# Performance work log

Hardware: AMD Instinct MI355X
Metric: run time of the kernel (lower is better)

Reference implementation:

```python
import jax, jax.numpy as jnp
import numpy as np

DIM = 512
NUM_HEADS = 8
HEAD_DIM = DIM // NUM_HEADS
GAMMA = 1.0


def setup_inputs() -> dict:
    key = jax.random.key(0)
    ks = jax.random.split(key, 10)
    B, S = 2, 2048
    x_real = jax.random.normal(ks[0], (B, S, DIM), dtype=jnp.float32)
    x_imag = jax.random.normal(ks[1], (B, S, DIM), dtype=jnp.float32)
    def xavier(k, fan_in, fan_out):
        lim = float(np.sqrt(6.0 / (fan_in + fan_out)))
        return jax.random.uniform(k, (fan_in, fan_out), jnp.float32, -lim, lim)
    # torch Linear(in,out): weight [out,in]; we store transposed [in,out]
    Wq = xavier(ks[2], 2 * DIM, DIM); bq = jnp.zeros((DIM,), jnp.float32)
    Wk = xavier(ks[3], 2 * DIM, DIM); bk = jnp.zeros((DIM,), jnp.float32)
    Wv = xavier(ks[4], 2 * DIM, DIM); bv = jnp.zeros((DIM,), jnp.float32)
    Wo = xavier(ks[5], DIM, 2 * DIM); bo = jnp.zeros((2 * DIM,), jnp.float32)
    return {"x_real": x_real, "x_imag": x_imag, "Wq": Wq, "bq": bq,
            "Wk": Wk, "bk": bk, "Wv": Wv, "bv": bv, "Wo": Wo, "bo": bo}


def reference(x_real, x_imag, Wq, bq, Wk, bk, Wv, bv, Wo, bo):
    B, S, _ = x_real.shape
    real_embed = jnp.concatenate([x_real, x_imag], axis=-1)  # [B,S,2*dim]
    def proj(W, b):
        y = real_embed @ W + b                               # [B,S,dim]
        return y.reshape(B, S, NUM_HEADS, HEAD_DIM).transpose(0, 2, 1, 3)  # [B,H,S,d]
    Q = proj(Wq, bq)
    K = proj(Wk, bk)
    V = proj(Wv, bv)
    # softmax over head_dim is broadcast-invariant, so the Bhattacharyya
    # coefficient sum_d sqrt(p_i[d]*q_j[d]) factorizes into a matmul.
    sp = jnp.sqrt(jax.nn.softmax(Q, axis=-1))  # [B,H,S,d]
    sq = jnp.sqrt(jax.nn.softmax(K, axis=-1))  # [B,H,S,d]
    bc = jnp.einsum('bhid,bhjd->bhij', sp, sq)  # Bhattacharyya coeff [B,H,S,S]
    bc = jnp.clip(bc, -1.0, 1.0)
    dist = jnp.arccos(bc)
    attn = jax.nn.softmax(-GAMMA * dist * dist, axis=-1)  # [B,H,S,S]
    attended = jnp.einsum('bhij,bhjd->bhid', attn, V)
    attended = attended.transpose(0, 2, 1, 3).reshape(B, S, DIM)
    out = attended @ Wo + bo  # [B,S,2*dim] = concat(real_out, imag_out)
    return out
```

## Files before the change

kernel.cpp:

```cpp
#include <hip/hip_runtime.h>
#include <math.h>


typedef __attribute__((ext_vector_type(8))) short short8;
typedef __attribute__((ext_vector_type(4))) short bf16x4;
typedef __attribute__((ext_vector_type(4))) float f32x4;

#define MFMA(a, b, c) __builtin_amdgcn_mfma_f32_16x16x32_bf16((a), (b), (c), 0, 0, 0)

static __device__ __forceinline__ short f2bf(float f) {
    unsigned u = __float_as_uint(f);
    u += 0x7fffu + ((u >> 16) & 1u);
    return (short)(u >> 16);
}

static __device__ __forceinline__ void gld_lds16(const short* g, short* l) {
    __builtin_amdgcn_global_load_lds(
        (const __attribute__((address_space(1))) unsigned int*)g,
        (__attribute__((address_space(3))) unsigned int*)l, 16, 0, 0);
}

__global__ __launch_bounds__(256) void convert_x(
    const float* __restrict__ xr, const float* __restrict__ xi,
    short* __restrict__ xb)
{
    int idx = blockIdx.x * 256 + threadIdx.x;
    int e = idx << 2;
    int m = e >> 10, k = e & 1023;
    const float* src = (k < 512) ? xr : xi;
    float4 t = *(const float4*)(src + (size_t)m * 512 + (k & 511));
    unsigned lo = (unsigned short)f2bf(t.x) | ((unsigned)(unsigned short)f2bf(t.y) << 16);
    unsigned hi = (unsigned short)f2bf(t.z) | ((unsigned)(unsigned short)f2bf(t.w) << 16);
    uint2 o; o.x = lo; o.y = hi;
    *(uint2*)(xb + e) = o;
}

__global__ __launch_bounds__(256) void transpose_w(
    const float* __restrict__ Wq, const float* __restrict__ Wk,
    const float* __restrict__ Wv, const float* __restrict__ Wo,
    short* __restrict__ wqt, short* __restrict__ wkt,
    short* __restrict__ wvt, short* __restrict__ wot)
{
    __shared__ float t[32][33];
    const int z = blockIdx.z;
    const float* src = (z == 0) ? Wq : (z == 1) ? Wk : (z == 2) ? Wv : Wo;
    short* dst = (z == 0) ? wqt : (z == 1) ? wkt : (z == 2) ? wvt : wot;
    const int K = (z < 3) ? 1024 : 512;
    const int N = (z < 3) ? 512 : 1024;
    const int n0 = blockIdx.x << 5, k0 = blockIdx.y << 5;
    if (n0 >= N || k0 >= K) return;
    const int tx = threadIdx.x & 31, ty = threadIdx.x >> 5;
    #pragma unroll
    for (int i = 0; i < 4; ++i)
        t[ty + 8 * i][tx] = src[(size_t)(k0 + ty + 8 * i) * N + n0 + tx];
    __syncthreads();
    #pragma unroll
    for (int i = 0; i < 4; ++i)
        dst[(size_t)(n0 + ty + 8 * i) * K + k0 + tx] = f2bf(t[tx][ty + 8 * i]);
}

__global__ __launch_bounds__(128, 4) void qkv_mfma(
    const short* __restrict__ xb, const short* __restrict__ wcat,
    const float* __restrict__ bq, const float* __restrict__ bk,
    const float* __restrict__ bv,
    short* __restrict__ sp, short* __restrict__ sq, short* __restrict__ vt)
{
    __shared__ short As[2][128 * 32];
    __shared__ short Bs[2][64 * 32];
    const int jb = blockIdx.x;
    const int m0 = blockIdx.y << 7;
    const int tid = threadIdx.x;
    const int w = tid >> 6, lane = tid & 63;
    const int l = lane & 15, quad = lane >> 4;

    const int srow = lane >> 2;
    const int sseg = (lane & 3) << 3;
    const short* gA = xb   + (size_t)(m0        + (w << 6) + srow) * 1024 + sseg;
    const short* gB = wcat + (size_t)((jb << 6) + (w << 5) + srow) * 1024 + sseg;

    #pragma unroll
    for (int t = 0; t < 4; ++t)
        gld_lds16(gA + t * 16 * 1024, &As[0][((w << 2) + t) << 9]);
    #pragma unroll
    for (int t = 0; t < 2; ++t)
        gld_lds16(gB + t * 16 * 1024, &Bs[0][((w << 1) + t) << 9]);
    __syncthreads();

    const f32x4 z4 = {0.f, 0.f, 0.f, 0.f};
    f32x4 acc[4][4];
    #pragma unroll
    for (int i = 0; i < 4; ++i)
        #pragma unroll
        for (int j = 0; j < 4; ++j) acc[i][j] = z4;

    for (int kt = 0; kt < 32; ++kt) {
        const int cb = kt & 1, nb = cb ^ 1;
        if (kt < 31) {
            const int k0 = (kt + 1) << 5;
            #pragma unroll
            for (int t = 0; t < 4; ++t)
                gld_lds16(gA + k0 + t * 16 * 1024, &As[nb][((w << 2) + t) << 9]);
            #pragma unroll
            for (int t = 0; t < 2; ++t)
                gld_lds16(gB + k0 + t * 16 * 1024, &Bs[nb][((w << 1) + t) << 9]);
        }
        const short* Al = &As[cb][(w << 6) << 5];
        const short* Bl = &Bs[cb][0];
        short8 af[4], bfr[4];
        #pragma unroll
        for (int i = 0; i < 4; ++i)
            af[i] = *(const short8*)(Al + (((i << 4) + l) << 5) + (quad << 3));
        #pragma unroll
        for (int j = 0; j < 4; ++j)
            bfr[j] = *(const short8*)(Bl + (((j << 4) + l) << 5) + (quad << 3));
        #pragma unroll
        for (int i = 0; i < 4; ++i)
            #pragma unroll
            for (int j = 0; j < 4; ++j)
                acc[i][j] = MFMA(af[i], bfr[j], acc[i][j]);
        __syncthreads();
    }

    const int op = jb >> 3;
    const int h  = jb & 7;

    if (op < 2) {
        short* dst = (op == 0) ? sp : sq;
        const float* bias = (op == 0) ? bq : bk;
        float bcol[4];
        #pragma unroll
        for (int nt = 0; nt < 4; ++nt) bcol[nt] = bias[(h << 6) + (nt << 4) + l];
        #pragma unroll
        for (int i = 0; i < 4; ++i) {
            #pragma unroll
            for (int reg = 0; reg < 4; ++reg) {
                const int r = m0 + (w << 6) + (i << 4) + (quad << 2) + reg;
                const int b = r >> 11, s = r & 2047;
                float v[4];
                #pragma unroll
                for (int nt = 0; nt < 4; ++nt) v[nt] = acc[i][nt][reg] + bcol[nt];
                float mx = fmaxf(fmaxf(v[0], v[1]), fmaxf(v[2], v[3]));
                #pragma unroll
                for (int msk = 1; msk < 16; msk <<= 1) mx = fmaxf(mx, __shfl_xor(mx, msk));
                float e[4], ssum = 0.f;
                #pragma unroll
                for (int nt = 0; nt < 4; ++nt) { e[nt] = __expf(v[nt] - mx); ssum += e[nt]; }
                #pragma unroll
                for (int msk = 1; msk < 16; msk <<= 1) ssum += __shfl_xor(ssum, msk);
                float inv = 1.0f / ssum;
                short* o = dst + ((size_t)((b << 3) + h) * 2048 + s) * 64 + l;
                #pragma unroll
                for (int nt = 0; nt < 4; ++nt)
                    o[nt << 4] = f2bf(sqrtf(e[nt] * inv));
            }
        }
    } else {
        float bcol[4];
        #pragma unroll
        for (int nt = 0; nt < 4; ++nt) bcol[nt] = bv[(h << 6) + (nt << 4) + l];
        #pragma unroll
        for (int i = 0; i < 4; ++i) {
            const int sb = m0 + (w << 6) + (i << 4) + (quad << 2);
            const int b = sb >> 11, s = sb & 2047;
            #pragma unroll
            for (int nt = 0; nt < 4; ++nt) {
                const int d = (nt << 4) + l;
                bf16x4 pk;
                #pragma unroll
                for (int reg = 0; reg < 4; ++reg)
                    pk[reg] = f2bf(acc[i][nt][reg] + bcol[nt]);
                *(bf16x4*)(vt + ((size_t)((b << 3) + h) * 64 + d) * 2048 + s) = pk;
            }
        }
    }
}

__global__ __launch_bounds__(256, 4) void attn_mfma(
    const short* __restrict__ sp, const short* __restrict__ sq,
    const short* __restrict__ vt, short* __restrict__ attB)
{
    __shared__ short sqT[2][64 * 72];
    __shared__ short vtT[2][64 * 72];
    __shared__ short Pb[4][16 * 72];
    __shared__ float denB[4][16];
    const int bh = blockIdx.y;
    const int m0 = blockIdx.x << 6;
    const int tid = threadIdx.x;
    const int w = tid >> 6, lane = tid & 63;
    const int l = lane & 15, quad = lane >> 4;

    const short* spB = sp + (size_t)bh * 2048 * 64;
    const short* sqB = sq + (size_t)bh * 2048 * 64;
    const short* vtB = vt + (size_t)bh * 64 * 2048;

    const short* apr = spB + (size_t)(m0 + w * 16 + l) * 64 + quad * 8;
    short8 aq0 = *(const short8*)(apr);
    short8 aq1 = *(const short8*)(apr + 32);

    const int srow = tid >> 2;
    const int scol = (tid & 3) * 16;
    const short* sqG = sqB + (size_t)srow * 64 + scol;
    const short* vtG = vtB + (size_t)srow * 2048 + scol;
    const int ldsOff = srow * 72 + scol;

    {
        short8 a0 = *(const short8*)(sqG);
        short8 a1 = *(const short8*)(sqG + 8);
        short8 b0 = *(const short8*)(vtG);
        short8 b1 = *(const short8*)(vtG + 8);
        *(short8*)(&sqT[0][ldsOff])     = a0;
        *(short8*)(&sqT[0][ldsOff + 8]) = a1;
        *(short8*)(&vtT[0][ldsOff])     = b0;
        *(short8*)(&vtT[0][ldsOff + 8]) = b1;
    }
    __syncthreads();

    const f32x4 z4 = {0.f, 0.f, 0.f, 0.f};
    f32x4 acc[4] = {z4, z4, z4, z4};
    float den = 0.f;
    short* Pw = &Pb[w][0];

    #pragma unroll 1
    for (int jt = 0; jt < 32; ++jt) {
        const int cb = jt & 1, nb = cb ^ 1;
        const int j0n = ((jt + 1) & 31) << 6;
        short8 na0 = *(const short8*)(sqG + (size_t)j0n * 64);
        short8 na1 = *(const short8*)(sqG + (size_t)j0n * 64 + 8);
        short8 nb0 = *(const short8*)(vtG + j0n);
        short8 nb1 = *(const short8*)(vtG + j0n + 8);

        const short* sqL = &sqT[cb][0];
        #pragma unroll
        for (int nt = 0; nt < 4; ++nt) {
            const short* ar = sqL + (nt * 16 + l) * 72 + quad * 8;
            short8 sa0 = *(const short8*)(ar);
            short8 sa1 = *(const short8*)(ar + 32);
            f32x4 p = MFMA(sa0, aq0, z4);
            p = MFMA(sa1, aq1, p);
            float wv[4];
            #pragma unroll
            for (int reg = 0; reg < 4; ++reg) {
                float u = fmaxf(1.0f - p[reg], 0.0f);
                float t = 0.000922f;
                t = fmaf(t, u, 0.00152228f);
                t = fmaf(t, u, 0.00384801f);
                t = fmaf(t, u, 0.01015873f);
                t = fmaf(t, u, 0.02857143f);
                t = fmaf(t, u, 0.08888889f);
                t = fmaf(t, u, 0.33333333f);
                t = fmaf(t, u, 2.0f);
                float e = __expf(-u * t);
                wv[reg] = e;
                den += e;
            }
            uint2 pk;
            pk.x = (__float_as_uint(wv[0]) >> 16) | (__float_as_uint(wv[1]) & 0xffff0000u);
            pk.y = (__float_as_uint(wv[2]) >> 16) | (__float_as_uint(wv[3]) & 0xffff0000u);
            *(uint2*)(&Pw[l * 72 + nt * 16 + quad * 4]) = pk;
        }

        const short* pr = Pw + l * 72 + quad * 8;
        short8 pa0 = *(const short8*)(pr);
        short8 pa1 = *(const short8*)(pr + 32);
        const short* vL = &vtT[cb][0];
        #pragma unroll
        for (int t4 = 0; t4 < 4; ++t4) {
            const short* vr = vL + (t4 * 16 + l) * 72 + quad * 8;
            short8 vb0 = *(const short8*)(vr);
            short8 vb1 = *(const short8*)(vr + 32);
            acc[t4] = MFMA(pa0, vb0, acc[t4]);
            acc[t4] = MFMA(pa1, vb1, acc[t4]);
        }

        *(short8*)(&sqT[nb][ldsOff])     = na0;
        *(short8*)(&sqT[nb][ldsOff + 8]) = na1;
        *(short8*)(&vtT[nb][ldsOff])     = nb0;
        *(short8*)(&vtT[nb][ldsOff + 8]) = nb1;
        __syncthreads();
    }

    den += __shfl_xor(den, 16);
    den += __shfl_xor(den, 32);
    if (lane < 16) denB[w][l] = den;
    float invd[4];
    #pragma unroll
    for (int reg = 0; reg < 4; ++reg)
        invd[reg] = 1.0f / denB[w][quad * 4 + reg];

    const int b = bh >> 3, hh = bh & 7;
    #pragma unroll
    for (int t4 = 0; t4 < 4; ++t4)
        #pragma unroll
        for (int reg = 0; reg < 4; ++reg) {
            const int row = m0 + w * 16 + quad * 4 + reg;
            attB[((size_t)(b * 2048 + row)) * 512 + hh * 64 + t4 * 16 + l] =
                f2bf(acc[t4][reg] * invd[reg]);
        }
}

__global__ __launch_bounds__(256, 3) void out_mfma(
    const short* __restrict__ attB, const short* __restrict__ wot,
    const float* __restrict__ bo, float* __restrict__ out)
{
    __shared__ short As[2][128 * 32];
    __shared__ short Bs[2][64 * 32];
    const int nb0 = blockIdx.x << 6;
    const int m0 = blockIdx.y << 7;
    const int tid = threadIdx.x;
    const int w = tid >> 6, lane = tid & 63;
    const int l = lane & 15, quad = lane >> 4;

    const short* gA = attB + (size_t)(m0  + (w << 4) + (lane >> 2)) * 512 + ((lane & 3) << 3);
    const short* gB = wot  + (size_t)(nb0 + (w << 4) + (lane >> 2)) * 512 + ((lane & 3) << 3);

    gld_lds16(gA,            &As[0][w << 9]);
    gld_lds16(gA + 64 * 512, &As[0][(w + 4) << 9]);
    gld_lds16(gB,            &Bs[0][w << 9]);
    __syncthreads();

    const f32x4 z4 = {0.f, 0.f, 0.f, 0.f};
    f32x4 acc[4][2];
    #pragma unroll
    for (int i = 0; i < 4; ++i) { acc[i][0] = z4; acc[i][1] = z4; }

    const int rsel = (w >> 1) << 6;
    const int csel = (w & 1) << 5;

    for (int kt = 0; kt < 16; ++kt) {
        const int cb = kt & 1, nbuf = cb ^ 1;
        if (kt < 15) {
            const int k0 = (kt + 1) << 5;
            gld_lds16(gA + k0,            &As[nbuf][w << 9]);
            gld_lds16(gA + k0 + 64 * 512, &As[nbuf][(w + 4) << 9]);
            gld_lds16(gB + k0,            &Bs[nbuf][w << 9]);
        }
        const short* Al = &As[cb][rsel << 5];
        const short* Bl = &Bs[cb][csel << 5];
        short8 af[4], bfr[2];
        #pragma unroll
        for (int i = 0; i < 4; ++i)
            af[i] = *(const short8*)(Al + (((i << 4) + l) << 5) + (quad << 3));
        #pragma unroll
        for (int j = 0; j < 2; ++j)
            bfr[j] = *(const short8*)(Bl + (((j << 4) + l) << 5) + (quad << 3));
        #pragma unroll
        for (int i = 0; i < 4; ++i) {
            acc[i][0] = MFMA(af[i], bfr[0], acc[i][0]);
            acc[i][1] = MFMA(af[i], bfr[1], acc[i][1]);
        }
        __syncthreads();
    }

    const int n0 = nb0 + csel;
    float bcol[2];
    bcol[0] = bo[n0 + l];
    bcol[1] = bo[n0 + 16 + l];
    #pragma unroll
    for (int i = 0; i < 4; ++i)
        #pragma unroll
        for (int reg = 0; reg < 4; ++reg) {
            const int m = m0 + rsel + (i << 4) + (quad << 2) + reg;
            float* o = out + (size_t)m * 1024 + n0 + l;
            o[0]  = acc[i][0][reg] + bcol[0];
            o[16] = acc[i][1][reg] + bcol[1];
        }
}

extern "C" void kernel_launch(void* const* d_in, const int* in_sizes, int n_in,
                              void* d_out, int out_size, void* d_ws, size_t ws_size,
                              hipStream_t stream) {
    const float* xr = (const float*)d_in[0];
    const float* xi = (const float*)d_in[1];
    const float* Wq = (const float*)d_in[2];
    const float* bq = (const float*)d_in[3];
    const float* Wk = (const float*)d_in[4];
    const float* bk = (const float*)d_in[5];
    const float* Wv = (const float*)d_in[6];
    const float* bv = (const float*)d_in[7];
    const float* Wo = (const float*)d_in[8];
    const float* bo = (const float*)d_in[9];
    float* out = (float*)d_out;

    short* base = (short*)d_ws;
    short* xb   = base;
    short* wqt  = xb  + 4194304;
    short* wkt  = wqt + 524288;
    short* wvt  = wkt + 524288;
    short* wot  = wvt + 524288;
    short* spW  = wot + 524288;
    short* sqW  = spW + 2097152;
    short* vtW  = sqW + 2097152;
    short* attB = vtW + 2097152;

    hipLaunchKernelGGL(convert_x, dim3(4096), dim3(256), 0, stream, xr, xi, xb);
    hipLaunchKernelGGL(transpose_w, dim3(32, 32, 4), dim3(256), 0, stream,
                       Wq, Wk, Wv, Wo, wqt, wkt, wvt, wot);
    hipLaunchKernelGGL(qkv_mfma, dim3(24, 32), dim3(128), 0, stream,
                       xb, wqt, bq, bk, bv, spW, sqW, vtW);
    hipLaunchKernelGGL(attn_mfma, dim3(32, 16), dim3(256), 0, stream,
                       spW, sqW, vtW, attB);
    hipLaunchKernelGGL(out_mfma, dim3(16, 32), dim3(256), 0, stream,
                       attB, wot, bo, out);
}
```

Measured before the change: 189.1 us.

## Swizzle attention LDS tiles, fold 1-p into MFMA, use packed f32 math

Replaces the padded (stride-72) shared-memory tiles with unpadded stride-64 tiles using an XOR swizzle on 16-byte chunks, shrinking LDS footprint while avoiding bank conflicts. It negates the query fragment and seeds the MFMA accumulator with ones so the MFMA directly produces 1-p, removing a subtraction. It also rewrites the arccos-squared polynomial and denominator accumulation in two-wide float vectors so the compiler can emit packed FP32 instructions. The swizzle must match between writes and reads, which adds index arithmetic and risk of subtle addressing errors.

```diff
diff --git a/kernel.cpp b/kernel.cpp
--- a/kernel.cpp
+++ b/kernel.cpp
@@ -5,6 +5,7 @@
 typedef __attribute__((ext_vector_type(8))) short short8;
 typedef __attribute__((ext_vector_type(4))) short bf16x4;
 typedef __attribute__((ext_vector_type(4))) float f32x4;
+typedef __attribute__((ext_vector_type(2))) float f32x2;
 
 #define MFMA(a, b, c) __builtin_amdgcn_mfma_f32_16x16x32_bf16((a), (b), (c), 0, 0, 0)
 
@@ -179,15 +180,16 @@
     const short* __restrict__ sp, const short* __restrict__ sq,
     const short* __restrict__ vt, short* __restrict__ attB)
 {
-    __shared__ short sqT[2][64 * 72];
-    __shared__ short vtT[2][64 * 72];
-    __shared__ short Pb[4][16 * 72];
+    __shared__ __align__(16) short sqT[2][64 * 64];
+    __shared__ __align__(16) short vtT[2][64 * 64];
+    __shared__ __align__(16) short Pb[4][16 * 64];
     __shared__ float denB[4][16];
     const int bh = blockIdx.y;
     const int m0 = blockIdx.x << 6;
     const int tid = threadIdx.x;
     const int w = tid >> 6, lane = tid & 63;
     const int l = lane & 15, quad = lane >> 4;
+    const int l7 = l & 7;
 
     const short* spB = sp + (size_t)bh * 2048 * 64;
     const short* sqB = sq + (size_t)bh * 2048 * 64;
@@ -196,28 +198,35 @@
     const short* apr = spB + (size_t)(m0 + w * 16 + l) * 64 + quad * 8;
     short8 aq0 = *(const short8*)(apr);
     short8 aq1 = *(const short8*)(apr + 32);
+    short8 nq0 = aq0 ^ (short)0x8000;
+    short8 nq1 = aq1 ^ (short)0x8000;
 
     const int srow = tid >> 2;
     const int scol = (tid & 3) * 16;
     const short* sqG = sqB + (size_t)srow * 64 + scol;
     const short* vtG = vtB + (size_t)srow * 2048 + scol;
-    const int ldsOff = srow * 72 + scol;
+    const int sl0 = (tid & 3) << 1;
+    const int sw0 = srow * 64 + (((sl0    ) ^ (srow & 7)) << 3);
+    const int sw1 = srow * 64 + (((sl0 | 1) ^ (srow & 7)) << 3);
+
+    const int sRd = (quad ^ l7) << 3;
 
     {
         short8 a0 = *(const short8*)(sqG);
         short8 a1 = *(const short8*)(sqG + 8);
         short8 b0 = *(const short8*)(vtG);
         short8 b1 = *(const short8*)(vtG + 8);
-        *(short8*)(&sqT[0][ldsOff])     = a0;
-        *(short8*)(&sqT[0][ldsOff + 8]) = a1;
-        *(short8*)(&vtT[0][ldsOff])     = b0;
-        *(short8*)(&vtT[0][ldsOff + 8]) = b1;
+        *(short8*)(&sqT[0][sw0]) = a0;
+        *(short8*)(&sqT[0][sw1]) = a1;
+        *(short8*)(&vtT[0][sw0]) = b0;
+        *(short8*)(&vtT[0][sw1]) = b1;
     }
     __syncthreads();
 
     const f32x4 z4 = {0.f, 0.f, 0.f, 0.f};
+    const f32x4 ones4 = {1.f, 1.f, 1.f, 1.f};
     f32x4 acc[4] = {z4, z4, z4, z4};
-    float den = 0.f;
+    f32x2 den2 = {0.f, 0.f};
     short* Pw = &Pb[w][0];
 
     #pragma unroll 1
@@ -232,53 +241,64 @@
         const short* sqL = &sqT[cb][0];
         #pragma unroll
         for (int nt = 0; nt < 4; ++nt) {
-            const short* ar = sqL + (nt * 16 + l) * 72 + quad * 8;
-            short8 sa0 = *(const short8*)(ar);
-            short8 sa1 = *(const short8*)(ar + 32);
-            f32x4 p = MFMA(sa0, aq0, z4);
-            p = MFMA(sa1, aq1, p);
-            float wv[4];
-            #pragma unroll
-            for (int reg = 0; reg < 4; ++reg) {
-                float u = fmaxf(1.0f - p[reg], 0.0f);
-                float t = 0.000922f;
-                t = fmaf(t, u, 0.00152228f);
-                t = fmaf(t, u, 0.00384801f);
-                t = fmaf(t, u, 0.01015873f);
-                t = fmaf(t, u, 0.02857143f);
-                t = fmaf(t, u, 0.08888889f);
-                t = fmaf(t, u, 0.33333333f);
-                t = fmaf(t, u, 2.0f);
-                float e = __expf(-u * t);
-                wv[reg] = e;
-                den += e;
-            }
+            const short* ar = sqL + ((nt * 16 + l) << 6);
+            short8 sa0 = *(const short8*)(ar + sRd);
+            short8 sa1 = *(const short8*)(ar + (sRd ^ 32));
+            f32x4 p = MFMA(sa0, nq0, ones4);
+            p = MFMA(sa1, nq1, p);
+            f32x2 u01 = {p[0], p[1]};
+            f32x2 u23 = {p[2], p[3]};
+            const f32x2 zz = {0.f, 0.f};
+#if __has_builtin(__builtin_elementwise_max)
+            u01 = __builtin_elementwise_max(u01, zz);
+            u23 = __builtin_elementwise_max(u23, zz);
+#else
+            u01.x = fmaxf(u01.x, 0.f); u01.y = fmaxf(u01.y, 0.f);
+            u23.x = fmaxf(u23.x, 0.f); u23.y = fmaxf(u23.y, 0.f);
+#endif
+            f32x2 t01 = {0.000922f, 0.000922f};
+            f32x2 t23 = t01;
+            t01 = t01 * u01 + 0.00152228f;  t23 = t23 * u23 + 0.00152228f;
+            t01 = t01 * u01 + 0.00384801f;  t23 = t23 * u23 + 0.00384801f;
+            t01 = t01 * u01 + 0.01015873f;  t23 = t23 * u23 + 0.01015873f;
+            t01 = t01 * u01 + 0.02857143f;  t23 = t23 * u23 + 0.02857143f;
+            t01 = t01 * u01 + 0.08888889f;  t23 = t23 * u23 + 0.08888889f;
+            t01 = t01 * u01 + 0.33333333f;  t23 = t23 * u23 + 0.33333333f;
+            t01 = t01 * u01 + 2.0f;         t23 = t23 * u23 + 2.0f;
+            f32x2 w01 = u01 * t01;
+            f32x2 w23 = u23 * t23;
+            float e0 = __expf(-w01.x), e1 = __expf(-w01.y);
+            float e2 = __expf(-w23.x), e3 = __expf(-w23.y);
+            f32x2 es = {e0 + e2, e1 + e3};
+            den2 += es;
             uint2 pk;
-            pk.x = (__float_as_uint(wv[0]) >> 16) | (__float_as_uint(wv[1]) & 0xffff0000u);
-            pk.y = (__float_as_uint(wv[2]) >> 16) | (__float_as_uint(wv[3]) & 0xffff0000u);
-            *(uint2*)(&Pw[l * 72 + nt * 16 + quad * 4]) = pk;
-        }
-
-        const short* pr = Pw + l * 72 + quad * 8;
-        short8 pa0 = *(const short8*)(pr);
-        short8 pa1 = *(const short8*)(pr + 32);
+            pk.x = (__float_as_uint(e0) >> 16) | (__float_as_uint(e1) & 0xffff0000u);
+            pk.y = (__float_as_uint(e2) >> 16) | (__float_as_uint(e3) & 0xffff0000u);
+            *(uint2*)(&Pw[(l << 6) + ((((nt << 1) + (quad >> 1)) ^ l7) << 3)
+                          + ((quad & 1) << 2)]) = pk;
+        }
+
+        const short* pr = Pw + (l << 6);
+        short8 pa0 = *(const short8*)(pr + sRd);
+        short8 pa1 = *(const short8*)(pr + (sRd ^ 32));
         const short* vL = &vtT[cb][0];
         #pragma unroll
         for (int t4 = 0; t4 < 4; ++t4) {
-            const short* vr = vL + (t4 * 16 + l) * 72 + quad * 8;
-            short8 vb0 = *(const short8*)(vr);
-            short8 vb1 = *(const short8*)(vr + 32);
+            const short* vr = vL + ((t4 * 16 + l) << 6);
+            short8 vb0 = *(const short8*)(vr + sRd);
+            short8 vb1 = *(const short8*)(vr + (sRd ^ 32));
             acc[t4] = MFMA(pa0, vb0, acc[t4]);
             acc[t4] = MFMA(pa1, vb1, acc[t4]);
         }
 
-        *(short8*)(&sqT[nb][ldsOff])     = na0;
-        *(short8*)(&sqT[nb][ldsOff + 8]) = na1;
-        *(short8*)(&vtT[nb][ldsOff])     = nb0;
-        *(short8*)(&vtT[nb][ldsOff + 8]) = nb1;
+        *(short8*)(&sqT[nb][sw0]) = na0;
+        *(short8*)(&sqT[nb][sw1]) = na1;
+        *(short8*)(&vtT[nb][sw0]) = nb0;
+        *(short8*)(&vtT[nb][sw1]) = nb1;
         __syncthreads();
     }
 
+    float den = den2.x + den2.y;
     den += __shfl_xor(den, 16);
     den += __shfl_xor(den, 32);
     if (lane < 16) denB[w][l] = den;
```

New measurement: 185.7 us. About the same (-1.8%).
